# Kernel optimization log

Measured on AMD Instinct MI355X. Metric: run time of the kernel, lower is better.

Reference implementation:

```python
import jax, jax.numpy as jnp
import numpy as np
from jax import lax

B, T, N, HID = 4, 144, 256, 64
CH, NC = 9, 4  # chunk_size_short, num_chunks_short


def setup_inputs():
    key = jax.random.key(0)
    ks = jax.random.split(key, 30)
    r = lambda i, sh, s=0.05: jax.random.normal(ks[i], sh, jnp.float32) * s
    adj = (jax.random.uniform(ks[1], (N, N)) < 0.1).astype(jnp.float32)
    adj = adj.at[jnp.arange(N), jnp.arange(N)].set(1.0)  # self-loops
    return {
        "seg": jax.random.normal(ks[0], (B, T, N, N), jnp.float32),
        "adj": adj,
        "dist": jax.random.uniform(ks[2], (N, N), jnp.float32),
        "W_gat": r(3, (N, HID)),
        "a_src": r(4, (HID,)),
        "a_dst": r(5, (HID,)),
        "lstm_Wih": r(6, (4 * HID, HID)),
        "lstm_Whh": r(7, (4 * HID, HID)),
        "lstm_bih": r(8, (4 * HID,)),
        "lstm_bhh": r(9, (4 * HID,)),
        "attnL_W": r(10, (HID, HID)),
        "attnL_b": r(11, (HID,)),
        "attnL_v": r(12, (HID,)),
        "gru_Wih": r(13, (NC, 3 * HID, HID)),
        "gru_Whh": r(14, (NC, 3 * HID, HID)),
        "gru_bih": r(15, (NC, 3 * HID)),
        "gru_bhh": r(16, (NC, 3 * HID)),
        "attnS_W": r(17, (NC, HID, HID)),
        "attnS_b": r(18, (NC, HID)),
        "attnS_v": r(19, (NC, HID)),
        "lin1_W": r(20, (2 * HID, HID + HID * NC)),
        "lin1_b": r(21, (2 * HID,)),
        "lin2_W": r(22, (N * N, 2 * HID)),
        "lin2_b": r(23, (N * N,)),
        "conv_k": r(24, (1, 1, 3, 3)),
        "conv_b": r(25, (1,)),
    }


def gat_features(seg, adj, dist, W_gat, a_src, a_dst):
    # Batches the per-timestep GAT over the time axis (B,T folded together).
    Wh = jnp.einsum('btnf,fh->btnh', seg, W_gat)                     # (B,T,N,H)
    e = jax.nn.leaky_relu((Wh @ a_src)[..., :, None] + (Wh @ a_dst)[..., None, :], 0.2)
    e = e - dist                                                     # distance penalty on logits
    logits = jnp.where(adj > 0, e, -1e9)                             # mask non-edges
    attn = jax.nn.softmax(logits, axis=-1)                           # (B,T,N,N)
    Hn = jax.nn.elu(jnp.einsum('btij,btjh->btih', attn, Wh))         # (B,T,N,H)
    return Hn.mean(axis=2)                                           # (B,T,H) mean-pool over nodes


def lstm(x, Wih, Whh, bih, bhh):
    h0 = jnp.zeros((x.shape[0], Whh.shape[1]), x.dtype)
    def step(carry, xt):
        h, c = carry
        g = xt @ Wih.T + bih + h @ Whh.T + bhh
        i, f, gg, o = jnp.split(g, 4, axis=-1)  # torch gate order i,f,g,o
        c = jax.nn.sigmoid(f) * c + jax.nn.sigmoid(i) * jnp.tanh(gg)
        h = jax.nn.sigmoid(o) * jnp.tanh(c)
        return (h, c), h
    _, ys = lax.scan(step, (h0, h0), jnp.swapaxes(x, 0, 1))
    return jnp.swapaxes(ys, 0, 1)


def gru(x, Wih, Whh, bih, bhh):
    h0 = jnp.zeros((x.shape[0], Whh.shape[1]), x.dtype)
    def step(h, xt):
        gx = xt @ Wih.T + bih
        gh = h @ Whh.T + bhh
        xr, xz, xn = jnp.split(gx, 3, axis=-1)  # torch gate order r,z,n
        hr, hz, hn = jnp.split(gh, 3, axis=-1)
        rr = jax.nn.sigmoid(xr + hr)
        zz = jax.nn.sigmoid(xz + hz)
        nn_ = jnp.tanh(xn + rr * hn)
        h = (1.0 - zz) * nn_ + zz * h
        return h, h
    _, ys = lax.scan(step, h0, jnp.swapaxes(x, 0, 1))
    return jnp.swapaxes(ys, 0, 1)


def tattn(h, W, b, v):
    s = jnp.tanh(h @ W + b) @ v          # (B,T) additive attention scores
    a = jax.nn.softmax(s, axis=1)
    return jnp.einsum('bt,bth->bh', a, h)


def reference(seg, adj, dist, W_gat, a_src, a_dst, lstm_Wih, lstm_Whh, lstm_bih, lstm_bhh,
              attnL_W, attnL_b, attnL_v, gru_Wih, gru_Whh, gru_bih, gru_bhh,
              attnS_W, attnS_b, attnS_v, lin1_W, lin1_b, lin2_W, lin2_b, conv_k, conv_b):
    Bsz = seg.shape[0]
    feats = gat_features(seg, adj, dist, W_gat, a_src, a_dst)        # (B,T,H)
    ctxL = tattn(lstm(feats, lstm_Wih, lstm_Whh, lstm_bih, lstm_bhh), attnL_W, attnL_b, attnL_v)
    # Short-term GCN features are the same GAT outputs on the last W_short steps.
    short = feats[:, -CH * NC:, :].reshape(Bsz, NC, CH, HID)
    gru_out = jax.vmap(gru, in_axes=(1, 0, 0, 0, 0), out_axes=1)(short, gru_Wih, gru_Whh, gru_bih, gru_bhh)
    ctxS = jax.vmap(tattn, in_axes=(1, 0, 0, 0), out_axes=1)(gru_out, attnS_W, attnS_b, attnS_v)  # (B,NC,H)
    fused = jnp.concatenate([ctxL, ctxS.reshape(Bsz, NC * HID)], axis=1)  # (B, 5H)
    h1 = jax.nn.relu(fused @ lin1_W.T + lin1_b)
    out = (h1 @ lin2_W.T + lin2_b).reshape(Bsz, 1, N, N)
    out = lax.conv_general_dilated(out, conv_k, (1, 1), 'SAME',
                                   dimension_numbers=('NCHW', 'OIHW', 'NCHW'))
    out = out + conv_b[None, :, None, None]
    return jax.nn.softplus(out[:, 0])
```

## Files before the change

kernel.cpp:

```cpp
#include <hip/hip_runtime.h>
#include <hip/hip_bf16.h>
#include <cstddef>


typedef __attribute__((ext_vector_type(8))) short bf16x8;
typedef __attribute__((ext_vector_type(4))) float f32x4;

__device__ __forceinline__ float sigf(float x) { return 1.0f / (1.0f + __expf(-x)); }
__device__ __forceinline__ float tanh_(float x) {
    x = fminf(fmaxf(x, -15.f), 15.f);
    float e = __expf(2.f * x);
    return (e - 1.f) / (e + 1.f);
}
__device__ __forceinline__ unsigned short f2b(float f) {
    unsigned u = __float_as_uint(f);
    u += 0x7FFFu + ((u >> 16) & 1u);
    return (unsigned short)(u >> 16);
}
__device__ __forceinline__ unsigned pk2(float lo, float hi) {
    __hip_bfloat162 h = __float22bfloat162_rn(float2{lo, hi});
    return *reinterpret_cast<unsigned*>(&h);
}
__device__ __forceinline__ float b2f(short s) {
    return __uint_as_float(((unsigned)(unsigned short)s) << 16);
}

__global__ void k_prep(const float* __restrict__ adj, const float* __restrict__ dist,
                       const float* __restrict__ W_gat,
                       unsigned short* __restrict__ Mb, unsigned short* __restrict__ Wt) {
    int blk = blockIdx.x, tid = threadIdx.x;
    if (blk < 256) {
        int i = blk * 256 + tid;
        Mb[i] = f2b((adj[i] > 0.f) ? -dist[i] : -1e9f);
    } else {
        for (int it = 0; it < 64; ++it) {
            int e = it * 256 + tid;
            int k = e >> 6, c = e & 63;
            Wt[c * 256 + k] = f2b(W_gat[e]);
        }
    }
}

__global__ __launch_bounds__(256, 6) void k_gatA(
    const float* __restrict__ seg, const unsigned short* __restrict__ Wt,
    const float* __restrict__ a_src, const float* __restrict__ a_dst,
    unsigned short* __restrict__ WhT, float* __restrict__ svec, float* __restrict__ dvec,
    float* __restrict__ smaxp, float* __restrict__ dmaxp) {
    __shared__ __align__(16) short A_s[64 * 64];
    __shared__ float red[8];

    const int tid  = threadIdx.x;
    const int lane = tid & 63;
    const int wv   = tid >> 6;
    const int blk  = blockIdx.x;
    const int bt   = blk >> 2;
    const int sub  = blk & 3;
    const float* __restrict__ segp = seg + (size_t)bt * 65536 + sub * 64 * 256;

    f32x4 acc[4];
    #pragma unroll
    for (int n = 0; n < 4; ++n) acc[n] = (f32x4)(0.f);

    for (int kc = 0; kc < 4; ++kc) {
        #pragma unroll
        for (int it = 0; it < 2; ++it) {
            int unit = it * 256 + tid;
            int row = unit >> 3, u = unit & 7;
            const float* g = segp + row * 256 + kc * 64 + u * 8;
            f32x4 v0 = *(const f32x4*)g;
            f32x4 v1 = *(const f32x4*)(g + 4);
            uint4 pk;
            pk.x = pk2(v0[0], v0[1]); pk.y = pk2(v0[2], v0[3]);
            pk.z = pk2(v1[0], v1[1]); pk.w = pk2(v1[2], v1[3]);
            *(uint4*)&A_s[(row * 8 + (u ^ (row & 7))) * 8] = pk;
        }
        bf16x8 bfr[2][4];
        #pragma unroll
        for (int kt2 = 0; kt2 < 2; ++kt2) {
            int ku = kt2 * 4 + (lane >> 4);
            #pragma unroll
            for (int nt = 0; nt < 4; ++nt) {
                int col = nt * 16 + (lane & 15);
                bfr[kt2][nt] = *(const bf16x8*)(Wt + col * 256 + kc * 64 + ku * 8);
            }
        }
        __syncthreads();
        int arow = wv * 16 + (lane & 15);
        #pragma unroll
        for (int kt2 = 0; kt2 < 2; ++kt2) {
            int ku = kt2 * 4 + (lane >> 4);
            bf16x8 afr = *(const bf16x8*)&A_s[(arow * 8 + (ku ^ (arow & 7))) * 8];
            #pragma unroll
            for (int nt = 0; nt < 4; ++nt)
                acc[nt] = __builtin_amdgcn_mfma_f32_16x16x32_bf16(afr, bfr[kt2][nt], acc[nt], 0, 0, 0);
        }
        __syncthreads();
    }

    float asv[4], adv[4];
    #pragma unroll
    for (int nt = 0; nt < 4; ++nt) {
        asv[nt] = a_src[nt * 16 + (lane & 15)];
        adv[nt] = a_dst[nt * 16 + (lane & 15)];
    }
    float mxs = -3e38f, mxd = -3e38f;
    int rowbase = sub * 64 + wv * 16;
    #pragma unroll
    for (int r = 0; r < 4; ++r) {
        float ps = acc[0][r] * asv[0] + acc[1][r] * asv[1] + acc[2][r] * asv[2] + acc[3][r] * asv[3];
        float pd = acc[0][r] * adv[0] + acc[1][r] * adv[1] + acc[2][r] * adv[2] + acc[3][r] * adv[3];
        #pragma unroll
        for (int m = 1; m < 16; m <<= 1) { ps += __shfl_xor(ps, m); pd += __shfl_xor(pd, m); }
        if ((lane & 15) == 0) {
            int row = rowbase + (lane >> 4) * 4 + r;
            svec[bt * 256 + row] = ps;
            dvec[bt * 256 + row] = pd;
        }
        mxs = fmaxf(mxs, ps); mxd = fmaxf(mxd, pd);
    }
    {
        unsigned short* Wp = WhT + (size_t)bt * 16384;
        int row0 = rowbase + (lane >> 4) * 4;
        #pragma unroll
        for (int nt = 0; nt < 4; ++nt) {
            int col = nt * 16 + (lane & 15);
            uint2 pk4;
            pk4.x = pk2(acc[nt][0], acc[nt][1]);
            pk4.y = pk2(acc[nt][2], acc[nt][3]);
            *(uint2*)(Wp + col * 256 + row0) = pk4;
        }
    }
    mxs = fmaxf(mxs, __shfl_xor(mxs, 16)); mxs = fmaxf(mxs, __shfl_xor(mxs, 32));
    mxd = fmaxf(mxd, __shfl_xor(mxd, 16)); mxd = fmaxf(mxd, __shfl_xor(mxd, 32));
    if (lane == 0) { red[wv] = mxs; red[4 + wv] = mxd; }
    __syncthreads();
    if (tid == 0) {
        smaxp[blk] = fmaxf(fmaxf(red[0], red[1]), fmaxf(red[2], red[3]));
        dmaxp[blk] = fmaxf(fmaxf(red[4], red[5]), fmaxf(red[6], red[7]));
    }
}

__global__ __launch_bounds__(256, 4) void k_gatB(
    const unsigned short* __restrict__ WhT, const float* __restrict__ svec,
    const float* __restrict__ dvec, const float* __restrict__ smaxp,
    const float* __restrict__ dmaxp, const unsigned short* __restrict__ Mb,
    float* __restrict__ fpart) {
    __shared__ __align__(16) float dv_l[256];
    __shared__ float red[256];

    const int tid  = threadIdx.x;
    const int lane = tid & 63;
    const int wv   = tid >> 6;
    const int blk  = blockIdx.x;
    const int bt   = blk >> 2;
    const int sub  = blk & 3;
    const unsigned short* __restrict__ Wp = WhT + (size_t)bt * 16384;

    dv_l[tid] = dvec[bt * 256 + tid];
    float mB;
    {
        float ms = fmaxf(fmaxf(smaxp[bt * 4], smaxp[bt * 4 + 1]),
                         fmaxf(smaxp[bt * 4 + 2], smaxp[bt * 4 + 3]));
        float md = fmaxf(fmaxf(dmaxp[bt * 4], dmaxp[bt * 4 + 1]),
                         fmaxf(dmaxp[bt * 4 + 2], dmaxp[bt * 4 + 3]));
        float x = ms + md;
        mB = fmaxf(x, 0.2f * x);
    }
    const int prow = sub * 64 + wv * 16 + (lane & 15);
    const float sv = svec[bt * 256 + prow];
    __syncthreads();

    f32x4 acc2[4];
    #pragma unroll
    for (int n = 0; n < 4; ++n) acc2[n] = (f32x4)(0.f);
    float psum = 0.f;
    const int jbase = (lane >> 4) * 8;

    #pragma unroll 1
    for (int kt = 0; kt < 8; ++kt) {
        int j0 = kt * 32 + jbase;
        bf16x8 bfr[4];
        #pragma unroll
        for (int nt = 0; nt < 4; ++nt) {
            int col = nt * 16 + (lane & 15);
            bfr[nt] = *(const bf16x8*)(Wp + col * 256 + j0);
        }
        bf16x8 mrow = *(const bf16x8*)(Mb + prow * 256 + j0);
        f32x4 d0 = *(const f32x4*)&dv_l[j0];
        f32x4 d1 = *(const f32x4*)&dv_l[j0 + 4];
        float p[8];
        #pragma unroll
        for (int e = 0; e < 4; ++e) {
            float u = sv + d0[e];
            u = fmaxf(u, 0.2f * u);
            p[e] = __expf(u + b2f(mrow[e]) - mB);
            float w = sv + d1[e];
            w = fmaxf(w, 0.2f * w);
            p[4 + e] = __expf(w + b2f(mrow[4 + e]) - mB);
        }
        psum += ((p[0] + p[1]) + (p[2] + p[3])) + ((p[4] + p[5]) + (p[6] + p[7]));
        uint4 upf;
        upf.x = pk2(p[0], p[1]); upf.y = pk2(p[2], p[3]);
        upf.z = pk2(p[4], p[5]); upf.w = pk2(p[6], p[7]);
        bf16x8 pf = *reinterpret_cast<bf16x8*>(&upf);
        #pragma unroll
        for (int nt = 0; nt < 4; ++nt)
            acc2[nt] = __builtin_amdgcn_mfma_f32_16x16x32_bf16(pf, bfr[nt], acc2[nt], 0, 0, 0);
    }
    psum += __shfl_xor(psum, 16);
    psum += __shfl_xor(psum, 32);

    float part[4] = {0.f, 0.f, 0.f, 0.f};
    #pragma unroll
    for (int r = 0; r < 4; ++r) {
        float rs  = __shfl(psum, ((lane >> 4) << 2) + r);
        float inv = 1.0f / rs;
        #pragma unroll
        for (int nt = 0; nt < 4; ++nt) {
            float x = acc2[nt][r] * inv;
            x = (x > 0.f) ? x : expm1f(x);
            part[nt] += x;
        }
    }
    #pragma unroll
    for (int nt = 0; nt < 4; ++nt) {
        part[nt] += __shfl_xor(part[nt], 16);
        part[nt] += __shfl_xor(part[nt], 32);
    }
    if ((lane >> 4) == 0) {
        #pragma unroll
        for (int nt = 0; nt < 4; ++nt) red[wv * 64 + nt * 16 + lane] = part[nt];
    }
    __syncthreads();
    if (tid < 64)
        fpart[blk * 64 + tid] = red[tid] + red[64 + tid] + red[128 + tid] + red[192 + tid];
}

__global__ __launch_bounds__(256) void k_feats(
    const float* __restrict__ fpart, const float* __restrict__ lWih,
    const float* __restrict__ lbih, const float* __restrict__ lbhh,
    float* __restrict__ feats, float* __restrict__ gx) {
    __shared__ __align__(16) float fl[64];
    int bt = blockIdx.x, tid = threadIdx.x;
    if (tid < 64) {
        float f = (fpart[(bt * 4 + 0) * 64 + tid] + fpart[(bt * 4 + 1) * 64 + tid]
                 + fpart[(bt * 4 + 2) * 64 + tid] + fpart[(bt * 4 + 3) * 64 + tid]) * (1.0f / 256.0f);
        feats[bt * 64 + tid] = f;
        fl[tid] = f;
    }
    __syncthreads();
    float a = lbih[tid] + lbhh[tid];
    const float* wp = lWih + tid * 64;
    #pragma unroll
    for (int k4 = 0; k4 < 16; ++k4) {
        f32x4 w = *(const f32x4*)(wp + k4 * 4);
        f32x4 x = *(const f32x4*)&fl[k4 * 4];
        a += w[0] * x[0] + w[1] * x[1] + w[2] * x[2] + w[3] * x[3];
    }
    gx[bt * 256 + tid] = a;
}

__global__ __launch_bounds__(256) void k_rnn(
    const float* __restrict__ gx, const float* __restrict__ lWhh, float* __restrict__ lout,
    const float* __restrict__ feats, const float* __restrict__ gWih,
    const float* __restrict__ gWhh, const float* __restrict__ gbih,
    const float* __restrict__ gbhh, float* __restrict__ gout) {
    int tid = threadIdx.x;
    if (blockIdx.x < 4) {
        int b = blockIdx.x;
        int lane = tid & 63, wv = tid >> 6;
        __shared__ __align__(16) float hv[4][64];
        __shared__ __align__(16) float gl[2][256];
        float wr[64];
        #pragma unroll
        for (int q = 0; q < 16; ++q)
            *(f32x4*)&wr[q * 4] = *(const f32x4*)&lWhh[tid * 64 + q * 4];
        float c_s = 0.f;
        hv[wv][lane] = 0.f;
        float gx_cur = gx[(size_t)b * 144 * 256 + tid];
        for (int t = 0; t < 144; ++t) {
            float gx_next = (t < 143) ? gx[((size_t)b * 144 + t + 1) * 256 + tid] : 0.f;
            float s0 = 0.f, s1 = 0.f, s2 = 0.f, s3 = 0.f;
            #pragma unroll
            for (int q = 0; q < 4; ++q) {
                f32x4 h0 = *(const f32x4*)&hv[wv][q * 16];
                f32x4 h1 = *(const f32x4*)&hv[wv][q * 16 + 4];
                f32x4 h2 = *(const f32x4*)&hv[wv][q * 16 + 8];
                f32x4 h3 = *(const f32x4*)&hv[wv][q * 16 + 12];
                s0 += wr[q*16+ 0]*h0[0] + wr[q*16+ 1]*h0[1] + wr[q*16+ 2]*h0[2] + wr[q*16+ 3]*h0[3];
                s1 += wr[q*16+ 4]*h1[0] + wr[q*16+ 5]*h1[1] + wr[q*16+ 6]*h1[2] + wr[q*16+ 7]*h1[3];
                s2 += wr[q*16+ 8]*h2[0] + wr[q*16+ 9]*h2[1] + wr[q*16+10]*h2[2] + wr[q*16+11]*h2[3];
                s3 += wr[q*16+12]*h3[0] + wr[q*16+13]*h3[1] + wr[q*16+14]*h3[2] + wr[q*16+15]*h3[3];
            }
            float a = gx_cur + ((s0 + s1) + (s2 + s3));
            gl[t & 1][tid] = a;
            __syncthreads();
            float ig = gl[t & 1][lane],       fg = gl[t & 1][64 + lane],
                  gg = gl[t & 1][128 + lane], og = gl[t & 1][192 + lane];
            c_s = sigf(fg) * c_s + sigf(ig) * tanh_(gg);
            float h = sigf(og) * tanh_(c_s);
            hv[wv][lane] = h;
            if (wv == 0) lout[(b * 144 + t) * 64 + lane] = h;
            gx_cur = gx_next;
        }
    } else {
        int bi_ = blockIdx.x - 4;
        int b = bi_ >> 2, c2 = bi_ & 3;
        __shared__ float hvg[64], xvg[64], gxl[192], ghl[192];
        float wi[64], wh[64], bi = 0.f, bh = 0.f, h_s = 0.f;
        if (tid < 192) {
            #pragma unroll
            for (int q = 0; q < 16; ++q) {
                *(f32x4*)&wi[q * 4] = *(const f32x4*)&gWih[(size_t)(c2 * 192 + tid) * 64 + q * 4];
                *(f32x4*)&wh[q * 4] = *(const f32x4*)&gWhh[(size_t)(c2 * 192 + tid) * 64 + q * 4];
            }
            bi = gbih[c2 * 192 + tid];
            bh = gbhh[c2 * 192 + tid];
        }
        if (tid < 64) hvg[tid] = 0.f;
        __syncthreads();
        for (int s = 0; s < 9; ++s) {
            int t = 108 + c2 * 9 + s;
            if (tid < 64) xvg[tid] = feats[(b * 144 + t) * 64 + tid];
            __syncthreads();
            if (tid < 192) {
                float ax = bi, ah = bh;
                float a0 = 0.f, a1 = 0.f, b0 = 0.f, b1 = 0.f;
                #pragma unroll
                for (int k = 0; k < 64; k += 2) {
                    a0 += wi[k] * xvg[k];     a1 += wi[k + 1] * xvg[k + 1];
                    b0 += wh[k] * hvg[k];     b1 += wh[k + 1] * hvg[k + 1];
                }
                gxl[tid] = ax + a0 + a1; ghl[tid] = ah + b0 + b1;
            }
            __syncthreads();
            if (tid < 64) {
                float xr = gxl[tid], xz = gxl[64 + tid], xn = gxl[128 + tid];
                float hr = ghl[tid], hz = ghl[64 + tid], hn = ghl[128 + tid];
                float rr = sigf(xr + hr), zz = sigf(xz + hz);
                float nn = tanh_(xn + rr * hn);
                h_s = (1.f - zz) * nn + zz * h_s;
                hvg[tid] = h_s;
                gout[((b * 4 + c2) * 9 + s) * 64 + tid] = h_s;
            }
            __syncthreads();
        }
    }
}

__global__ __launch_bounds__(256) void k_ctx(
    const float* __restrict__ lout, const float* __restrict__ aLW,
    const float* __restrict__ aLb, const float* __restrict__ aLv,
    const float* __restrict__ gout, const float* __restrict__ aSW,
    const float* __restrict__ aSb, const float* __restrict__ aSv,
    float* __restrict__ ctxL, float* __restrict__ ctxS) {
    int tid = threadIdx.x;
    if (blockIdx.x < 4) {
        int b = blockIdx.x;
        int wv = tid >> 6, lane = tid & 63;
        __shared__ __align__(16) float Hl[144 * 64];
        __shared__ float sc[144];
        __shared__ float al[144];
        for (int i = tid; i < 9216; i += 256) Hl[i] = lout[b * 9216 + i];
        float wcol[64];
        #pragma unroll
        for (int k = 0; k < 64; ++k) wcol[k] = aLW[k * 64 + lane];
        float bb = aLb[lane], vv = aLv[lane];
        __syncthreads();
        for (int g = 0; g < 36; ++g) {
            int t = g * 4 + wv;
            float acc = bb;
            #pragma unroll
            for (int q = 0; q < 16; ++q) {
                f32x4 h4 = *(const f32x4*)&Hl[t * 64 + q * 4];
                acc += wcol[q * 4 + 0] * h4[0] + wcol[q * 4 + 1] * h4[1]
                     + wcol[q * 4 + 2] * h4[2] + wcol[q * 4 + 3] * h4[3];
            }
            float p = tanh_(acc) * vv;
            #pragma unroll
            for (int m = 1; m < 64; m <<= 1) p += __shfl_xor(p, m);
            if (lane == 0) sc[t] = p;
        }
        __syncthreads();
        float mx = -3e38f;
        for (int t2 = 0; t2 < 144; ++t2) mx = fmaxf(mx, sc[t2]);
        float ss = 0.f;
        for (int t2 = 0; t2 < 144; ++t2) ss += __expf(sc[t2] - mx);
        float inv = 1.f / ss;
        if (tid < 144) al[tid] = __expf(sc[tid] - mx) * inv;
        __syncthreads();
        if (tid < 64) {
            float acc = 0.f;
            for (int t2 = 0; t2 < 144; ++t2) acc += al[t2] * Hl[t2 * 64 + tid];
            ctxL[b * 64 + tid] = acc;
        }
    } else {
        int bi_ = blockIdx.x - 4;
        int b = bi_ >> 2, c2 = bi_ & 3;
        __shared__ float xv2[64];
        if (tid < 64) {
            int lane = tid;
            const float* Wc = aSW + c2 * 4096;
            float wcol[64];
            #pragma unroll
            for (int k = 0; k < 64; ++k) wcol[k] = Wc[k * 64 + lane];
            float bb = aSb[c2 * 64 + lane], vv = aSv[c2 * 64 + lane];
            float sv[9], hl[9];
            #pragma unroll 1
            for (int s = 0; s < 9; ++s) {
                float h = gout[((size_t)((b * 4 + c2) * 9 + s)) * 64 + lane];
                hl[s] = h;
                xv2[lane] = h;
                float acc = bb;
                #pragma unroll
                for (int k = 0; k < 64; ++k) acc += wcol[k] * xv2[k];
                float p = tanh_(acc) * vv;
                #pragma unroll
                for (int m = 1; m < 64; m <<= 1) p += __shfl_xor(p, m);
                sv[s] = p;
            }
            float mx = -3e38f;
            #pragma unroll
            for (int s = 0; s < 9; ++s) mx = fmaxf(mx, sv[s]);
            float ss = 0.f;
            #pragma unroll
            for (int s = 0; s < 9; ++s) { sv[s] = __expf(sv[s] - mx); ss += sv[s]; }
            float inv = 1.f / ss;
            float acc = 0.f;
            #pragma unroll
            for (int s = 0; s < 9; ++s) acc += sv[s] * inv * hl[s];
            ctxS[(b * 4 + c2) * 64 + lane] = acc;
        }
    }
}

__global__ __launch_bounds__(512) void k_lin1(
    const float* __restrict__ ctxL, const float* __restrict__ ctxS,
    const float* __restrict__ W, const float* __restrict__ bb,
    float* __restrict__ h1) {
    int tid = threadIdx.x;
    __shared__ __align__(16) float fu[4 * 320];
    for (int c = tid; c < 1280; c += 512) {
        int b2 = c / 320, k = c % 320;
        fu[c] = (k < 64) ? ctxL[b2 * 64 + k] : ctxS[b2 * 256 + (k - 64)];
    }
    __syncthreads();
    int b = tid >> 7, r = tid & 127;
    float acc = bb[r];
    #pragma unroll 4
    for (int k4 = 0; k4 < 80; ++k4) {
        f32x4 w = *(const f32x4*)&W[r * 320 + k4 * 4];
        f32x4 x = *(const f32x4*)&fu[b * 320 + k4 * 4];
        acc += w[0] * x[0] + w[1] * x[1] + w[2] * x[2] + w[3] * x[3];
    }
    h1[b * 128 + r] = fmaxf(acc, 0.f);
}

__global__ __launch_bounds__(256) void k_lin2(
    const float* __restrict__ h1, const float* __restrict__ W,
    const float* __restrict__ bb, float* __restrict__ h2) {
    __shared__ __align__(16) float h1l[512];
    int tid = threadIdx.x, blk = blockIdx.x;
    for (int c = tid; c < 512; c += 256) h1l[c] = h1[c];
    __syncthreads();
    int r = blk * 64 + (tid >> 2);
    int q = tid & 3;
    const float* wp = W + (size_t)r * 128 + q * 32;
    float a0 = 0.f, a1 = 0.f, a2 = 0.f, a3 = 0.f;
    #pragma unroll
    for (int i = 0; i < 8; ++i) {
        f32x4 w  = *(const f32x4*)(wp + i * 4);
        f32x4 x0 = *(const f32x4*)&h1l[q * 32 + i * 4];
        f32x4 x1 = *(const f32x4*)&h1l[128 + q * 32 + i * 4];
        f32x4 x2 = *(const f32x4*)&h1l[256 + q * 32 + i * 4];
        f32x4 x3 = *(const f32x4*)&h1l[384 + q * 32 + i * 4];
        a0 += w[0] * x0[0] + w[1] * x0[1] + w[2] * x0[2] + w[3] * x0[3];
        a1 += w[0] * x1[0] + w[1] * x1[1] + w[2] * x1[2] + w[3] * x1[3];
        a2 += w[0] * x2[0] + w[1] * x2[1] + w[2] * x2[2] + w[3] * x2[3];
        a3 += w[0] * x3[0] + w[1] * x3[1] + w[2] * x3[2] + w[3] * x3[3];
    }
    a0 += __shfl_xor(a0, 1); a0 += __shfl_xor(a0, 2);
    a1 += __shfl_xor(a1, 1); a1 += __shfl_xor(a1, 2);
    a2 += __shfl_xor(a2, 1); a2 += __shfl_xor(a2, 2);
    a3 += __shfl_xor(a3, 1); a3 += __shfl_xor(a3, 2);
    if (q == 0) {
        float bv = bb[r];
        h2[r]             = a0 + bv;
        h2[65536 + r]     = a1 + bv;
        h2[2 * 65536 + r] = a2 + bv;
        h2[3 * 65536 + r] = a3 + bv;
    }
}

__global__ __launch_bounds__(256) void k_conv(
    const float* __restrict__ h2, const float* __restrict__ ck,
    const float* __restrict__ cb, float* __restrict__ out) {
    int x = threadIdx.x;
    int b = blockIdx.x >> 8, y = blockIdx.x & 255;
    float kk[9];
    #pragma unroll
    for (int i = 0; i < 9; ++i) kk[i] = ck[i];
    const float* base = h2 + b * 65536;
    float acc = cb[0];
    #pragma unroll
    for (int dy = -1; dy <= 1; ++dy) {
        int yy = y + dy;
        if (yy < 0 || yy > 255) continue;
        #pragma unroll
        for (int dx = -1; dx <= 1; ++dx) {
            int xx = x + dx;
            if (xx < 0 || xx > 255) continue;
            acc += base[yy * 256 + xx] * kk[(dy + 1) * 3 + (dx + 1)];
        }
    }
    float r = (acc > 20.f) ? acc : log1pf(__expf(acc));
    out[b * 65536 + y * 256 + x] = r;
}

extern "C" void kernel_launch(void* const* d_in, const int* in_sizes, int n_in,
                              void* d_out, int out_size, void* d_ws, size_t ws_size,
                              hipStream_t stream) {
    const float* seg   = (const float*)d_in[0];
    const float* adj   = (const float*)d_in[1];
    const float* dist  = (const float*)d_in[2];
    const float* W_gat = (const float*)d_in[3];
    const float* a_src = (const float*)d_in[4];
    const float* a_dst = (const float*)d_in[5];
    const float* lWih  = (const float*)d_in[6];
    const float* lWhh  = (const float*)d_in[7];
    const float* lbih  = (const float*)d_in[8];
    const float* lbhh  = (const float*)d_in[9];
    const float* aLW   = (const float*)d_in[10];
    const float* aLb   = (const float*)d_in[11];
    const float* aLv   = (const float*)d_in[12];
    const float* gWih  = (const float*)d_in[13];
    const float* gWhh  = (const float*)d_in[14];
    const float* gbih  = (const float*)d_in[15];
    const float* gbhh  = (const float*)d_in[16];
    const float* aSW   = (const float*)d_in[17];
    const float* aSb   = (const float*)d_in[18];
    const float* aSv   = (const float*)d_in[19];
    const float* l1W   = (const float*)d_in[20];
    const float* l1b   = (const float*)d_in[21];
    const float* l2W   = (const float*)d_in[22];
    const float* l2b   = (const float*)d_in[23];
    const float* ck    = (const float*)d_in[24];
    const float* cb    = (const float*)d_in[25];
    float* out = (float*)d_out;

    float* ws = (float*)d_ws;
    unsigned short* Mb  = (unsigned short*)ws;
    unsigned short* Wt  = (unsigned short*)(ws + 32768);
    float* svec  = ws + 40960;
    float* dvec  = svec + 147456;
    float* smaxp = dvec + 147456;
    float* dmaxp = smaxp + 2304;
    unsigned short* WhT = (unsigned short*)(dmaxp + 2304);
    float* fpart = dmaxp + 2304 + 4718592;
    float* feats = fpart + 147456;
    float* gx    = feats + 36864;
    float* lout  = gx + 147456;
    float* gout  = lout + 36864;
    float* ctxL  = gout + 9216;
    float* ctxS  = ctxL + 256;
    float* h1    = ctxS + 1024;
    float* h2    = h1 + 512;

    k_prep<<<257, 256, 0, stream>>>(adj, dist, W_gat, Mb, Wt);
    k_gatA<<<2304, 256, 0, stream>>>(seg, Wt, a_src, a_dst, WhT, svec, dvec, smaxp, dmaxp);
    k_gatB<<<2304, 256, 0, stream>>>(WhT, svec, dvec, smaxp, dmaxp, Mb, fpart);
    k_feats<<<576, 256, 0, stream>>>(fpart, lWih, lbih, lbhh, feats, gx);
    k_rnn<<<20, 256, 0, stream>>>(gx, lWhh, lout, feats, gWih, gWhh, gbih, gbhh, gout);
    k_ctx<<<20, 256, 0, stream>>>(lout, aLW, aLb, aLv, gout, aSW, aSb, aSv, ctxL, ctxS);
    k_lin1<<<1, 512, 0, stream>>>(ctxL, ctxS, l1W, l1b, h1);
    k_lin2<<<1024, 256, 0, stream>>>(h1, l2W, l2b, h2);
    k_conv<<<1024, 256, 0, stream>>>(h2, ck, cb, out);
}
```

Before: 272.1 us.

## Store WhT in MFMA fragment order and use readlane broadcast in LSTM

```diff
diff --git a/kernel.cpp b/kernel.cpp
--- a/kernel.cpp
+++ b/kernel.cpp
@@ -23,6 +23,9 @@
 }
 __device__ __forceinline__ float b2f(short s) {
     return __uint_as_float(((unsigned)(unsigned short)s) << 16);
+}
+__device__ __forceinline__ float rlane(float v, int k) {
+    return __uint_as_float(__builtin_amdgcn_readlane(__float_as_uint(v), k));
 }
 
 __global__ void k_prep(const float* __restrict__ adj, const float* __restrict__ dist,
@@ -118,22 +121,31 @@
         }
         mxs = fmaxf(mxs, ps); mxd = fmaxf(mxd, pd);
     }
+    mxs = fmaxf(mxs, __shfl_xor(mxs, 16)); mxs = fmaxf(mxs, __shfl_xor(mxs, 32));
+    mxd = fmaxf(mxd, __shfl_xor(mxd, 16)); mxd = fmaxf(mxd, __shfl_xor(mxd, 32));
+    if (lane == 0) { red[wv] = mxs; red[4 + wv] = mxd; }
+
     {
-        unsigned short* Wp = WhT + (size_t)bt * 16384;
-        int row0 = rowbase + (lane >> 4) * 4;
+        int c = lane & 15, q = lane >> 4;
+        int kt2  = wv >> 1;
+        int oct  = (wv & 1) * 2 + (q >> 1);
+        int laneP = oct * 16 + c;
+        int e0b  = (q & 1) * 8;
         #pragma unroll
         for (int nt = 0; nt < 4; ++nt) {
-            int col = nt * 16 + (lane & 15);
             uint2 pk4;
             pk4.x = pk2(acc[nt][0], acc[nt][1]);
             pk4.y = pk2(acc[nt][2], acc[nt][3]);
-            *(uint2*)(Wp + col * 256 + row0) = pk4;
-        }
-    }
-    mxs = fmaxf(mxs, __shfl_xor(mxs, 16)); mxs = fmaxf(mxs, __shfl_xor(mxs, 32));
-    mxd = fmaxf(mxd, __shfl_xor(mxd, 16)); mxd = fmaxf(mxd, __shfl_xor(mxd, 32));
-    if (lane == 0) { red[wv] = mxs; red[4 + wv] = mxd; }
+            *(uint2*)((char*)A_s + (((kt2 * 4 + nt) * 64 + laneP) * 16 + e0b)) = pk4;
+        }
+    }
     __syncthreads();
+    {
+        const uint4* Fs = (const uint4*)A_s;
+        uint4* Gd = (uint4*)(WhT + (size_t)bt * 16384 + sub * 4096);
+        Gd[tid] = Fs[tid];
+        Gd[256 + tid] = Fs[256 + tid];
+    }
     if (tid == 0) {
         smaxp[blk] = fmaxf(fmaxf(red[0], red[1]), fmaxf(red[2], red[3]));
         dmaxp[blk] = fmaxf(fmaxf(red[4], red[5]), fmaxf(red[6], red[7]));
@@ -181,10 +193,8 @@
         int j0 = kt * 32 + jbase;
         bf16x8 bfr[4];
         #pragma unroll
-        for (int nt = 0; nt < 4; ++nt) {
-            int col = nt * 16 + (lane & 15);
-            bfr[nt] = *(const bf16x8*)(Wp + col * 256 + j0);
-        }
+        for (int nt = 0; nt < 4; ++nt)
+            bfr[nt] = *(const bf16x8*)(Wp + ((kt * 4 + nt) * 64 + lane) * 8);
         bf16x8 mrow = *(const bf16x8*)(Mb + prow * 256 + j0);
         f32x4 d0 = *(const f32x4*)&dv_l[j0];
         f32x4 d1 = *(const f32x4*)&dv_l[j0 + 4];
@@ -268,29 +278,24 @@
     int tid = threadIdx.x;
     if (blockIdx.x < 4) {
         int b = blockIdx.x;
-        int lane = tid & 63, wv = tid >> 6;
-        __shared__ __align__(16) float hv[4][64];
+        int lane = tid & 63;
         __shared__ __align__(16) float gl[2][256];
         float wr[64];
         #pragma unroll
         for (int q = 0; q < 16; ++q)
             *(f32x4*)&wr[q * 4] = *(const f32x4*)&lWhh[tid * 64 + q * 4];
         float c_s = 0.f;
-        hv[wv][lane] = 0.f;
-        float gx_cur = gx[(size_t)b * 144 * 256 + tid];
+        float hprev = 0.f;
+        float gx_cur = gx[(size_t)b * 36864 + tid];
         for (int t = 0; t < 144; ++t) {
             float gx_next = (t < 143) ? gx[((size_t)b * 144 + t + 1) * 256 + tid] : 0.f;
             float s0 = 0.f, s1 = 0.f, s2 = 0.f, s3 = 0.f;
             #pragma unroll
-            for (int q = 0; q < 4; ++q) {
-                f32x4 h0 = *(const f32x4*)&hv[wv][q * 16];
-                f32x4 h1 = *(const f32x4*)&hv[wv][q * 16 + 4];
-                f32x4 h2 = *(const f32x4*)&hv[wv][q * 16 + 8];
-                f32x4 h3 = *(const f32x4*)&hv[wv][q * 16 + 12];
-                s0 += wr[q*16+ 0]*h0[0] + wr[q*16+ 1]*h0[1] + wr[q*16+ 2]*h0[2] + wr[q*16+ 3]*h0[3];
-                s1 += wr[q*16+ 4]*h1[0] + wr[q*16+ 5]*h1[1] + wr[q*16+ 6]*h1[2] + wr[q*16+ 7]*h1[3];
-                s2 += wr[q*16+ 8]*h2[0] + wr[q*16+ 9]*h2[1] + wr[q*16+10]*h2[2] + wr[q*16+11]*h2[3];
-                s3 += wr[q*16+12]*h3[0] + wr[q*16+13]*h3[1] + wr[q*16+14]*h3[2] + wr[q*16+15]*h3[3];
+            for (int k = 0; k < 64; k += 4) {
+                s0 += wr[k]     * rlane(hprev, k);
+                s1 += wr[k + 1] * rlane(hprev, k + 1);
+                s2 += wr[k + 2] * rlane(hprev, k + 2);
+                s3 += wr[k + 3] * rlane(hprev, k + 3);
             }
             float a = gx_cur + ((s0 + s1) + (s2 + s3));
             gl[t & 1][tid] = a;
@@ -299,8 +304,8 @@
                   gg = gl[t & 1][128 + lane], og = gl[t & 1][192 + lane];
             c_s = sigf(fg) * c_s + sigf(ig) * tanh_(gg);
             float h = sigf(og) * tanh_(c_s);
-            hv[wv][lane] = h;
-            if (wv == 0) lout[(b * 144 + t) * 64 + lane] = h;
+            hprev = h;
+            if (tid < 64) lout[(b * 144 + t) * 64 + lane] = h;
             gx_cur = gx_next;
         }
     } else {
```

After: 231.4 us. 1.18x faster.
